# Optimization experiments

Measured on AMD Instinct MI355X. Metric: run time of the kernel, lower is better.

## Reference

```python
import jax, jax.numpy as jnp
import numpy as np

NEMBEDS = 512
EMBED_DIM = 64


def setup_inputs() -> dict:
    key = jax.random.key(0)
    k1, k2 = jax.random.split(key)
    z_e = jax.random.normal(k1, (32, EMBED_DIM, 64, 64), dtype=jnp.float32)
    codebook = jax.random.uniform(
        k2, (NEMBEDS, EMBED_DIM), dtype=jnp.float32,
        minval=-1.0 / NEMBEDS, maxval=1.0 / NEMBEDS)
    return {"z_e": z_e, "codebook": codebook}


def reference(z_e, codebook):
    # NCHW -> NHWC, flatten spatial+batch into tokens
    z = jnp.transpose(z_e, (0, 2, 3, 1))          # [B,H,W,D]
    B, H, W, D = z.shape
    flat = z.reshape(-1, D)                        # [N,D]
    # squared L2 distances (argmin of ||.||_2 == argmin of ||.||_2^2)
    # expanded form avoids the [N,K,D] broadcast intermediate
    d2 = (jnp.sum(flat * flat, axis=-1, keepdims=True)
          - 2.0 * flat @ codebook.T
          + jnp.sum(codebook * codebook, axis=-1))  # [N,K]
    inds = jnp.argmin(d2, axis=1)                   # [N]
    # direct gather == one-hot matmul lookup
    z_q = codebook[inds].reshape(B, H, W, D)        # [B,H,W,D]
    # commitment + codebook loss, per-batch mean over H,W,D
    sg = jax.lax.stop_gradient
    vq_loss = (jnp.mean((sg(z) - z_q) ** 2, axis=(1, 2, 3))
               + 0.25 * jnp.mean((z - sg(z_q)) ** 2, axis=(1, 2, 3)))  # [B]
    # straight-through estimator
    z_q_st = z + sg(z_q - z)
    out = jnp.transpose(z_q_st, (0, 3, 1, 2))       # back to NCHW
    return out, vq_loss, inds[:, None]
```

## Files before the change

kernel.cpp:

```cpp
#include <hip/hip_runtime.h>

#define NEMB 512
#define DIM 64
#define NB 32
#define HW 4096
#define NTOK (NB * HW)
#define TPB 256
#define TOKBLK 256
#define BLOCKS (NTOK / TOKBLK)

typedef float f32x16 __attribute__((ext_vector_type(16)));
typedef short bf16x8 __attribute__((ext_vector_type(8)));

#define WS_PART 0
#define WS_SUMC 512
#define WS_CMAXP 1024
#define WS_SCMAXP 1032
#define WS_CH 1040

__device__ __forceinline__ unsigned short f2bf(float f) {
    unsigned u = __float_as_uint(f);
    unsigned r = u + 0x7FFFu + ((u >> 16) & 1u);
    return (unsigned short)(r >> 16);
}
__device__ __forceinline__ float bf2f(unsigned short h) {
    return __uint_as_float((unsigned)h << 16);
}

__global__ void vq_prep(const float* __restrict__ cb, float* __restrict__ ws)
{
    const int tid = threadIdx.x;
    const int k   = blockIdx.x * 64 + tid;

    float sc_v;
    {
#pragma clang fp contract(off)
        float s = 0.f;
#pragma unroll
        for (int d = 0; d < DIM; ++d) {
            float v = cb[k * DIM + d];
            float p = v * v;
            s = s + p;
        }
        sc_v = s;
        ws[WS_SUMC + k] = s;
    }

    float cmax_t = 0.f;
    unsigned* chp = (unsigned*)(ws + WS_CH) + k * 32;
#pragma unroll
    for (int q = 0; q < 32; ++q) {
        float v0 = cb[k * DIM + 2 * q], v1 = cb[k * DIM + 2 * q + 1];
        cmax_t = fmaxf(cmax_t, fmaxf(fabsf(v0), fabsf(v1)));
        unsigned short h0 = f2bf(v0), h1 = f2bf(v1);
        chp[q] = (unsigned)h0 | ((unsigned)h1 << 16);
    }

    float cm = cmax_t, sm = sc_v;
#pragma unroll
    for (int off = 32; off; off >>= 1) {
        cm = fmaxf(cm, __shfl_xor(cm, off));
        sm = fmaxf(sm, __shfl_xor(sm, off));
    }
    if (tid == 0) {
        ws[WS_CMAXP  + blockIdx.x] = cm;
        ws[WS_SCMAXP + blockIdx.x] = sm;
    }
}

__global__ __launch_bounds__(TPB, 2)
void vq_main(const float* __restrict__ z_e, const float* __restrict__ cb,
             const float* __restrict__ ws, float* __restrict__ out,
             float* __restrict__ loss_part, float* __restrict__ inds_out)
{
    __shared__ uint4 ch_s[NEMB * 9];
    __shared__ float sumc_s[NEMB];
    __shared__ float red_s[TPB];
    __shared__ float sc2[2];

    const int tid  = threadIdx.x;
    const int gid  = blockIdx.x;
    const int b    = gid >> 4;
    const int base = (gid & 15) * TOKBLK;
    const int w    = tid >> 6;
    const int l    = tid & 63;
    const int col  = l & 31;
    const int half = l >> 5;

    {
        const uint4* chg = (const uint4*)(ws + WS_CH);
#pragma unroll
        for (int i = 0; i < 16; ++i) {
            int idx = i * TPB + tid;
            int c = idx >> 3, bd = idx & 7;
            int slot = (bd + c) & 7;
            ch_s[c * 9 + slot] = chg[idx];
        }
        sumc_s[tid]       = ws[WS_SUMC + tid];
        sumc_s[tid + TPB] = ws[WS_SUMC + tid + TPB];
        if (tid == 0) {
            float cm = ws[WS_CMAXP], sm = ws[WS_SCMAXP];
#pragma unroll
            for (int i = 1; i < 8; ++i) {
                cm = fmaxf(cm, ws[WS_CMAXP + i]);
                sm = fmaxf(sm, ws[WS_SCMAXP + i]);
            }
            sc2[0] = cm; sc2[1] = sm;
        }
    }

    const float* zb = z_e + (size_t)b * DIM * HW;
    const int t0 = base + w * 64;
    uint4 bzh[2][4], bzl[2][4];
    float l1p[2] = {0.f, 0.f}, szp[2] = {0.f, 0.f};
#pragma unroll
    for (int tt = 0; tt < 2; ++tt) {
        int tok = t0 + tt * 32 + col;
#pragma unroll
        for (int ks = 0; ks < 4; ++ks) {
            unsigned hh[8], ll[8];
#pragma unroll
            for (int j = 0; j < 8; ++j) {
                int d = 16 * ks + 8 * half + j;
                float v = zb[(size_t)d * HW + tok];
                l1p[tt] += fabsf(v);
                szp[tt] = fmaf(v, v, szp[tt]);
                unsigned short h = f2bf(v);
                unsigned short lo = f2bf(v - bf2f(h));
                hh[j] = h; ll[j] = lo;
            }
            bzh[tt][ks] = make_uint4(hh[0] | (hh[1] << 16), hh[2] | (hh[3] << 16),
                                     hh[4] | (hh[5] << 16), hh[6] | (hh[7] << 16));
            bzl[tt][ks] = make_uint4(ll[0] | (ll[1] << 16), ll[2] | (ll[3] << 16),
                                     ll[4] | (ll[5] << 16), ll[6] | (ll[7] << 16));
        }
    }
    float L1[2], SZ[2];
#pragma unroll
    for (int tt = 0; tt < 2; ++tt) {
        L1[tt] = l1p[tt] + __shfl_xor(l1p[tt], 32);
        SZ[tt] = szp[tt] + __shfl_xor(szp[tt], 32);
    }
    __syncthreads();

    const float cmax = sc2[0], scmax = sc2[1];
    float gapd[2];
#pragma unroll
    for (int tt = 0; tt < 2; ++tt)
        gapd[tt] = 8.0e-3f * cmax * L1[tt] + 0.5f * scmax + 1.2e-7f * SZ[tt] + 1e-6f;

    unsigned mask0[8], mask1[8];
#pragma unroll
    for (int i = 0; i < 8; ++i) { mask0[i] = 0u; mask1[i] = 0u; }
    float runm[2] = {-3.402823466e38f, -3.402823466e38f};

    for (int ct = 0; ct < 16; ++ct) {
        bf16x8 ah[4];
        const int c = 32 * ct + col;
        const int rowb = c * 9;
#pragma unroll
        for (int ks = 0; ks < 4; ++ks) {
            int slot = ((2 * ks + half) + c) & 7;
            uint4 u1 = ch_s[rowb + slot];
            ah[ks] = *(bf16x8*)&u1;
        }
#pragma unroll
        for (int tt = 0; tt < 2; ++tt) {
            f32x16 acc = {0.f, 0.f, 0.f, 0.f, 0.f, 0.f, 0.f, 0.f,
                          0.f, 0.f, 0.f, 0.f, 0.f, 0.f, 0.f, 0.f};
#pragma unroll
            for (int ks = 0; ks < 4; ++ks)
                acc = __builtin_amdgcn_mfma_f32_32x32x16_bf16(ah[ks], *(bf16x8*)&bzh[tt][ks], acc, 0, 0, 0);
#pragma unroll
            for (int ks = 0; ks < 4; ++ks)
                acc = __builtin_amdgcn_mfma_f32_32x32x16_bf16(ah[ks], *(bf16x8*)&bzl[tt][ks], acc, 0, 0, 0);
            float m = acc[0];
#pragma unroll
            for (int r = 1; r < 16; ++r) m = fmaxf(m, acc[r]);
            float rm = fmaxf(tt == 0 ? runm[0] : runm[1], m);
            if (tt == 0) runm[0] = rm; else runm[1] = rm;
            float thr = rm - (tt == 0 ? gapd[0] : gapd[1]);
            unsigned bits = 0;
#pragma unroll
            for (int r = 0; r < 16; ++r)
                bits |= (acc[r] >= thr) ? (1u << r) : 0u;
            unsigned sh = bits << ((ct & 1) * 16);
            if (tt == 0) mask0[ct >> 1] |= sh; else mask1[ct >> 1] |= sh;
        }
    }

    unsigned om[8], xm[8];
#pragma unroll
    for (int i = 0; i < 8; ++i) {
        om[i] = half ? mask1[i] : mask0[i];
        xm[i] = __shfl_xor(half ? mask0[i] : mask1[i], 32);
    }

    const int hwme = base + tid;
    float z[DIM];
    float sumz;
    {
#pragma clang fp contract(off)
        sumz = 0.f;
#pragma unroll
        for (int d = 0; d < DIM; ++d) {
            float v = zb[(size_t)d * HW + hwme];
            z[d] = v;
            float p = v * v;
            sumz = sumz + p;
        }
    }

    float best = 3.402823466e38f;
    int bk = 0;
    for (int ct = 0; ct < 16; ++ct) {
        unsigned A = (om[ct >> 1] >> ((ct & 1) * 16)) & 0xFFFFu;
        unsigned B = (xm[ct >> 1] >> ((ct & 1) * 16)) & 0xFFFFu;
        unsigned wo = ((A & 0xFu)) | (((A >> 4) & 0xFu) << 8) |
                      (((A >> 8) & 0xFu) << 16) | (((A >> 12) & 0xFu) << 24);
        unsigned wx = ((B & 0xFu)) | (((B >> 4) & 0xFu) << 8) |
                      (((B >> 8) & 0xFu) << 16) | (((B >> 12) & 0xFu) << 24);
        unsigned wc = half ? ((wo << 4) | wx) : (wo | (wx << 4));
        while (wc) {
            int kk = __builtin_ctz(wc);
            wc &= wc - 1;
            int k = 32 * ct + kk;
            const float4* c4 = (const float4*)(cb + (size_t)k * DIM);
            float a0 = 0.f;
#pragma unroll
            for (int g = 0; g < DIM / 4; ++g) {
                float4 u = c4[g];
                a0 = fmaf(z[4 * g + 0], u.x, a0);
                a0 = fmaf(z[4 * g + 1], u.y, a0);
                a0 = fmaf(z[4 * g + 2], u.z, a0);
                a0 = fmaf(z[4 * g + 3], u.w, a0);
            }
            float d2 = (sumz - 2.0f * a0) + sumc_s[k];
            if (d2 < best) { best = d2; bk = k; }
        }
    }

    inds_out[(size_t)gid * TOKBLK + tid] = (float)bk;
    float* ob = out + (size_t)b * DIM * HW;
    float lsum = 0.f;
    const float4* q4 = (const float4*)(cb + (size_t)bk * DIM);
    {
#pragma clang fp contract(off)
#pragma unroll
        for (int g = 0; g < DIM / 4; ++g) {
            float4 qq = q4[g];
            float qv[4] = {qq.x, qq.y, qq.z, qq.w};
#pragma unroll
            for (int j = 0; j < 4; ++j) {
                int d = g * 4 + j;
                float t1 = qv[j] - z[d];
                ob[(size_t)d * HW + hwme] = z[d] + t1;
                float p = t1 * t1;
                lsum = lsum + p;
            }
        }
    }

    __syncthreads();
    red_s[tid] = lsum;
    __syncthreads();
#pragma unroll
    for (int s = 128; s > 0; s >>= 1) {
        if (tid < s) red_s[tid] = red_s[tid] + red_s[tid + s];
        __syncthreads();
    }
    if (tid == 0) loss_part[gid] = red_s[0];
}

__global__ void vq_loss_final(const float* __restrict__ part,
                              float* __restrict__ loss_out)
{
    int b = threadIdx.x;
    if (b < NB) {
        float s = 0.f;
        for (int i = 0; i < 16; ++i)
            s = s + part[b * 16 + i];
        float m = s * (1.0f / (HW * DIM));
        loss_out[b] = m + 0.25f * m;
    }
}

extern "C" void kernel_launch(void* const* d_in, const int* in_sizes, int n_in,
                              void* d_out, int out_size, void* d_ws, size_t ws_size,
                              hipStream_t stream)
{
    const float* z_e = (const float*)d_in[0];
    const float* cb  = (const float*)d_in[1];

    float* out  = (float*)d_out;
    float* loss = out + (size_t)NB * DIM * HW;
    float* inds = loss + NB;
    float* ws   = (float*)d_ws;

    vq_prep<<<8, 64, 0, stream>>>(cb, ws);
    vq_main<<<BLOCKS, TPB, 0, stream>>>(z_e, cb, ws, out, ws + WS_PART, inds);
    vq_loss_final<<<1, 64, 0, stream>>>(ws + WS_PART, loss);
}
```

Measured before the change: 85.39 us.

## Drop bf16 low-part split of tokens and read codebook fragments directly from global

```diff
diff --git a/kernel.cpp b/kernel.cpp
--- a/kernel.cpp
+++ b/kernel.cpp
@@ -23,9 +23,6 @@
     unsigned r = u + 0x7FFFu + ((u >> 16) & 1u);
     return (unsigned short)(r >> 16);
 }
-__device__ __forceinline__ float bf2f(unsigned short h) {
-    return __uint_as_float((unsigned)h << 16);
-}
 
 __global__ void vq_prep(const float* __restrict__ cb, float* __restrict__ ws)
 {
@@ -47,13 +44,20 @@
     }
 
     float cmax_t = 0.f;
-    unsigned* chp = (unsigned*)(ws + WS_CH) + k * 32;
-#pragma unroll
-    for (int q = 0; q < 32; ++q) {
-        float v0 = cb[k * DIM + 2 * q], v1 = cb[k * DIM + 2 * q + 1];
-        cmax_t = fmaxf(cmax_t, fmaxf(fabsf(v0), fabsf(v1)));
-        unsigned short h0 = f2bf(v0), h1 = f2bf(v1);
-        chp[q] = (unsigned)h0 | ((unsigned)h1 << 16);
+    uint4* chf = (uint4*)(ws + WS_CH);
+    const int ct  = k >> 5;
+    const int col = k & 31;
+#pragma unroll
+    for (int bd = 0; bd < 8; ++bd) {
+        unsigned wd[4];
+#pragma unroll
+        for (int q = 0; q < 4; ++q) {
+            float v0 = cb[k * DIM + 8 * bd + 2 * q];
+            float v1 = cb[k * DIM + 8 * bd + 2 * q + 1];
+            cmax_t = fmaxf(cmax_t, fmaxf(fabsf(v0), fabsf(v1)));
+            wd[q] = (unsigned)f2bf(v0) | ((unsigned)f2bf(v1) << 16);
+        }
+        chf[(ct * 8 + bd) * 32 + col] = make_uint4(wd[0], wd[1], wd[2], wd[3]);
     }
 
     float cm = cmax_t, sm = sc_v;
@@ -73,7 +77,6 @@
              const float* __restrict__ ws, float* __restrict__ out,
              float* __restrict__ loss_part, float* __restrict__ inds_out)
 {
-    __shared__ uint4 ch_s[NEMB * 9];
     __shared__ float sumc_s[NEMB];
     __shared__ float red_s[TPB];
     __shared__ float sc2[2];
@@ -87,52 +90,38 @@
     const int col  = l & 31;
     const int half = l >> 5;
 
-    {
-        const uint4* chg = (const uint4*)(ws + WS_CH);
-#pragma unroll
-        for (int i = 0; i < 16; ++i) {
-            int idx = i * TPB + tid;
-            int c = idx >> 3, bd = idx & 7;
-            int slot = (bd + c) & 7;
-            ch_s[c * 9 + slot] = chg[idx];
-        }
-        sumc_s[tid]       = ws[WS_SUMC + tid];
-        sumc_s[tid + TPB] = ws[WS_SUMC + tid + TPB];
-        if (tid == 0) {
-            float cm = ws[WS_CMAXP], sm = ws[WS_SCMAXP];
-#pragma unroll
-            for (int i = 1; i < 8; ++i) {
-                cm = fmaxf(cm, ws[WS_CMAXP + i]);
-                sm = fmaxf(sm, ws[WS_SCMAXP + i]);
-            }
-            sc2[0] = cm; sc2[1] = sm;
-        }
+    sumc_s[tid]       = ws[WS_SUMC + tid];
+    sumc_s[tid + TPB] = ws[WS_SUMC + tid + TPB];
+    if (tid == 0) {
+        float cm = ws[WS_CMAXP], sm = ws[WS_SCMAXP];
+#pragma unroll
+        for (int i = 1; i < 8; ++i) {
+            cm = fmaxf(cm, ws[WS_CMAXP + i]);
+            sm = fmaxf(sm, ws[WS_SCMAXP + i]);
+        }
+        sc2[0] = cm; sc2[1] = sm;
     }
 
     const float* zb = z_e + (size_t)b * DIM * HW;
     const int t0 = base + w * 64;
-    uint4 bzh[2][4], bzl[2][4];
+    uint4 bzh[2][4];
     float l1p[2] = {0.f, 0.f}, szp[2] = {0.f, 0.f};
 #pragma unroll
     for (int tt = 0; tt < 2; ++tt) {
         int tok = t0 + tt * 32 + col;
 #pragma unroll
         for (int ks = 0; ks < 4; ++ks) {
-            unsigned hh[8], ll[8];
+            unsigned hh[8];
 #pragma unroll
             for (int j = 0; j < 8; ++j) {
                 int d = 16 * ks + 8 * half + j;
                 float v = zb[(size_t)d * HW + tok];
                 l1p[tt] += fabsf(v);
                 szp[tt] = fmaf(v, v, szp[tt]);
-                unsigned short h = f2bf(v);
-                unsigned short lo = f2bf(v - bf2f(h));
-                hh[j] = h; ll[j] = lo;
+                hh[j] = f2bf(v);
             }
             bzh[tt][ks] = make_uint4(hh[0] | (hh[1] << 16), hh[2] | (hh[3] << 16),
                                      hh[4] | (hh[5] << 16), hh[6] | (hh[7] << 16));
-            bzl[tt][ks] = make_uint4(ll[0] | (ll[1] << 16), ll[2] | (ll[3] << 16),
-                                     ll[4] | (ll[5] << 16), ll[6] | (ll[7] << 16));
         }
     }
     float L1[2], SZ[2];
@@ -147,8 +136,9 @@
     float gapd[2];
 #pragma unroll
     for (int tt = 0; tt < 2; ++tt)
-        gapd[tt] = 8.0e-3f * cmax * L1[tt] + 0.5f * scmax + 1.2e-7f * SZ[tt] + 1e-6f;
-
+        gapd[tt] = 1.6e-2f * cmax * L1[tt] + 0.5f * scmax + 1.2e-7f * SZ[tt] + 1e-6f;
+
+    const uint4* chf = (const uint4*)(ws + WS_CH);
     unsigned mask0[8], mask1[8];
 #pragma unroll
     for (int i = 0; i < 8; ++i) { mask0[i] = 0u; mask1[i] = 0u; }
@@ -156,12 +146,9 @@
 
     for (int ct = 0; ct < 16; ++ct) {
         bf16x8 ah[4];
-        const int c = 32 * ct + col;
-        const int rowb = c * 9;
 #pragma unroll
         for (int ks = 0; ks < 4; ++ks) {
-            int slot = ((2 * ks + half) + c) & 7;
-            uint4 u1 = ch_s[rowb + slot];
+            uint4 u1 = chf[(ct * 8 + 2 * ks + half) * 32 + col];
             ah[ks] = *(bf16x8*)&u1;
         }
 #pragma unroll
@@ -171,9 +158,6 @@
 #pragma unroll
             for (int ks = 0; ks < 4; ++ks)
                 acc = __builtin_amdgcn_mfma_f32_32x32x16_bf16(ah[ks], *(bf16x8*)&bzh[tt][ks], acc, 0, 0, 0);
-#pragma unroll
-            for (int ks = 0; ks < 4; ++ks)
-                acc = __builtin_amdgcn_mfma_f32_32x32x16_bf16(ah[ks], *(bf16x8*)&bzl[tt][ks], acc, 0, 0, 0);
             float m = acc[0];
 #pragma unroll
             for (int r = 1; r < 16; ++r) m = fmaxf(m, acc[r]);
```

Measured after the change: 99.96 us. 1.17x slower.

## Drop bf16 low-part MFMA pass and build B operands via wave shuffles

Applied to the files above, without the earlier changes.

```diff
diff --git a/kernel.cpp b/kernel.cpp
--- a/kernel.cpp
+++ b/kernel.cpp
@@ -23,9 +23,6 @@
     unsigned r = u + 0x7FFFu + ((u >> 16) & 1u);
     return (unsigned short)(r >> 16);
 }
-__device__ __forceinline__ float bf2f(unsigned short h) {
-    return __uint_as_float((unsigned)h << 16);
-}
 
 __global__ void vq_prep(const float* __restrict__ cb, float* __restrict__ ws)
 {
@@ -82,7 +79,6 @@
     const int gid  = blockIdx.x;
     const int b    = gid >> 4;
     const int base = (gid & 15) * TOKBLK;
-    const int w    = tid >> 6;
     const int l    = tid & 63;
     const int col  = l & 31;
     const int half = l >> 5;
@@ -110,36 +106,49 @@
     }
 
     const float* zb = z_e + (size_t)b * DIM * HW;
-    const int t0 = base + w * 64;
-    uint4 bzh[2][4], bzl[2][4];
-    float l1p[2] = {0.f, 0.f}, szp[2] = {0.f, 0.f};
+    const int hwme = base + tid;
+    float z[DIM];
+    float sumz;
+    {
+#pragma clang fp contract(off)
+        sumz = 0.f;
+#pragma unroll
+        for (int d = 0; d < DIM; ++d) {
+            float v = zb[(size_t)d * HW + hwme];
+            z[d] = v;
+            float p = v * v;
+            sumz = sumz + p;
+        }
+    }
+    float l1own = 0.f, szown = 0.f;
+#pragma unroll
+    for (int d = 0; d < DIM; ++d) {
+        l1own += fabsf(z[d]);
+        szown = fmaf(z[d], z[d], szown);
+    }
+
+    uint4 bzh[2][4];
 #pragma unroll
     for (int tt = 0; tt < 2; ++tt) {
-        int tok = t0 + tt * 32 + col;
+        int src = tt * 32 + col;
 #pragma unroll
         for (int ks = 0; ks < 4; ++ks) {
-            unsigned hh[8], ll[8];
+            unsigned hh[8];
 #pragma unroll
             for (int j = 0; j < 8; ++j) {
-                int d = 16 * ks + 8 * half + j;
-                float v = zb[(size_t)d * HW + tok];
-                l1p[tt] += fabsf(v);
-                szp[tt] = fmaf(v, v, szp[tt]);
-                unsigned short h = f2bf(v);
-                unsigned short lo = f2bf(v - bf2f(h));
-                hh[j] = h; ll[j] = lo;
+                float vlo = __shfl(z[16 * ks + j],     src);
+                float vhi = __shfl(z[16 * ks + 8 + j], src);
+                hh[j] = f2bf(half ? vhi : vlo);
             }
             bzh[tt][ks] = make_uint4(hh[0] | (hh[1] << 16), hh[2] | (hh[3] << 16),
                                      hh[4] | (hh[5] << 16), hh[6] | (hh[7] << 16));
-            bzl[tt][ks] = make_uint4(ll[0] | (ll[1] << 16), ll[2] | (ll[3] << 16),
-                                     ll[4] | (ll[5] << 16), ll[6] | (ll[7] << 16));
         }
     }
     float L1[2], SZ[2];
 #pragma unroll
     for (int tt = 0; tt < 2; ++tt) {
-        L1[tt] = l1p[tt] + __shfl_xor(l1p[tt], 32);
-        SZ[tt] = szp[tt] + __shfl_xor(szp[tt], 32);
+        L1[tt] = __shfl(l1own, tt * 32 + col);
+        SZ[tt] = __shfl(szown, tt * 32 + col);
     }
     __syncthreads();
 
@@ -147,7 +156,7 @@
     float gapd[2];
 #pragma unroll
     for (int tt = 0; tt < 2; ++tt)
-        gapd[tt] = 8.0e-3f * cmax * L1[tt] + 0.5f * scmax + 1.2e-7f * SZ[tt] + 1e-6f;
+        gapd[tt] = 1.6e-2f * cmax * L1[tt] + 0.5f * scmax + 1.2e-7f * SZ[tt] + 1e-6f;
 
     unsigned mask0[8], mask1[8];
 #pragma unroll
@@ -171,9 +180,6 @@
 #pragma unroll
             for (int ks = 0; ks < 4; ++ks)
                 acc = __builtin_amdgcn_mfma_f32_32x32x16_bf16(ah[ks], *(bf16x8*)&bzh[tt][ks], acc, 0, 0, 0);
-#pragma unroll
-            for (int ks = 0; ks < 4; ++ks)
-                acc = __builtin_amdgcn_mfma_f32_32x32x16_bf16(ah[ks], *(bf16x8*)&bzl[tt][ks], acc, 0, 0, 0);
             float m = acc[0];
 #pragma unroll
             for (int r = 1; r < 16; ++r) m = fmaxf(m, acc[r]);
@@ -194,21 +200,6 @@
     for (int i = 0; i < 8; ++i) {
         om[i] = half ? mask1[i] : mask0[i];
         xm[i] = __shfl_xor(half ? mask0[i] : mask1[i], 32);
-    }
-
-    const int hwme = base + tid;
-    float z[DIM];
-    float sumz;
-    {
-#pragma clang fp contract(off)
-        sumz = 0.f;
-#pragma unroll
-        for (int d = 0; d < DIM; ++d) {
-            float v = zb[(size_t)d * HW + hwme];
-            z[d] = v;
-            float p = v * v;
-            sumz = sumz + p;
-        }
     }
 
     float best = 3.402823466e38f;
```

After: 90.13 us. 5.5% more time.
